# Kernel tuning notes

Measured on AMD Instinct MI355X. Metric: run time of the kernel, lower is better.

Reference implementation:

```python
import jax, jax.numpy as jnp
import numpy as np
from jax import lax

N, D, K = 8192, 512, 16
EPS = 1e-8


def _safe_sqrt(x):
    # sqrt with a guard so vjp is finite at exact zeros (diagonal of dist matrix)
    return jnp.where(x > 0, jnp.sqrt(jnp.maximum(x, 1e-12)), 0.0)


def _pairwise_dist(a):
    # [n, d] -> [n, n] euclidean distances via Gram trick
    sq = jnp.sum(a * a, axis=-1)
    d2 = sq[:, None] + sq[None, :] - 2.0 * (a @ a.T)
    return _safe_sqrt(d2)


def _curvature_proxy(emb, k):
    n = emb.shape[0]
    dists = _pairwise_dist(emb)  # [n, n]
    neg_d, knn_idx = lax.top_k(-dists, k + 1)  # k+1 smallest
    knn_dists = -neg_d[:, 1:]   # drop self [n, k]
    knn_idx = knn_idx[:, 1:]    # [n, k]
    avg_dist_to_neighbors = knn_dists.mean(axis=1)  # [n]

    nb = emb[knn_idx]  # [n, k, d] gathered neighbor embeddings
    nsq = jnp.sum(nb * nb, axis=-1)  # [n, k]
    gram = jnp.einsum('nkd,nld->nkl', nb, nb)  # [n, k, k]
    inter = _safe_sqrt(nsq[:, :, None] + nsq[:, None, :] - 2.0 * gram)

    mask = jnp.triu(jnp.ones((k, k), dtype=bool), 1)
    n_pairs = k * (k - 1) // 2
    inter_mean = jnp.sum(jnp.where(mask, inter, 0.0), axis=(1, 2)) / n_pairs  # [n]

    curvature = inter_mean / (avg_dist_to_neighbors + EPS)
    return curvature, knn_dists


def setup_inputs() -> dict:
    key = jax.random.key(0)
    k1, k2, k3 = jax.random.split(key, 3)
    embeddings = jax.random.normal(k1, (N, D), dtype=jnp.float32)
    ref_curvature = jax.random.uniform(k2, (N,), dtype=jnp.float32)
    ref_distances = jax.random.uniform(k3, (N, K), dtype=jnp.float32)
    return {"embeddings": embeddings, "ref_curvature": ref_curvature,
            "ref_distances": ref_distances}


def reference(embeddings, ref_curvature, ref_distances):
    curr_curv, curr_dists = _curvature_proxy(embeddings, K)
    curvature_loss = jnp.mean((curr_curv - ref_curvature) ** 2)
    scale_loss = (curr_dists.mean() - ref_distances.mean()) ** 2
    return curvature_loss + 0.1 * scale_loss
```

## Files before the change

### kernel.cpp

```cpp
#include <hip/hip_runtime.h>
#include <cfloat>
#include <cmath>
#include <stdint.h>

#define N 8192
#define D 512
#define K 16
#define RB 64
#define JS 2048
#define NSL (N / JS)
#define JT 128
#define KC 64
#define NCH (D / KC)
#define CAP 32
#define PB 64

typedef __bf16 bf16x8 __attribute__((ext_vector_type(8)));
typedef __bf16 bf16x4 __attribute__((ext_vector_type(4)));
typedef float  f32x16 __attribute__((ext_vector_type(16)));
typedef float  f32x4  __attribute__((ext_vector_type(4)));

__global__ __launch_bounds__(256)
void k_cast_sqnorm(const float* __restrict__ emb, float* __restrict__ sq,
                   __bf16* __restrict__ embh) {
    int row = blockIdx.x * 4 + (threadIdx.x >> 6);
    int lane = threadIdx.x & 63;
    const float4* e = (const float4*)(emb + (size_t)row * D);
    float s = 0.f;
    #pragma unroll
    for (int c = 0; c < 2; c++) {
        float4 v = e[lane + 64 * c];
        s += v.x * v.x + v.y * v.y + v.z * v.z + v.w * v.w;
        bf16x4 h = { (__bf16)v.x, (__bf16)v.y, (__bf16)v.z, (__bf16)v.w };
        *(bf16x4*)&embh[(size_t)row * D + (size_t)(lane + 64 * c) * 4] = h;
    }
    for (int off = 32; off; off >>= 1) s += __shfl_down(s, off, 64);
    if (lane == 0) sq[row] = s;
}

__global__ __launch_bounds__(512)
void k_knn(const __bf16* __restrict__ embh, const float* __restrict__ sq,
           float* __restrict__ pd2, int* __restrict__ pidx) {
    __shared__ __align__(16) __bf16 As[2][RB][KC + 8];
    __shared__ __align__(16) __bf16 Bs[2][JT][KC + 8];
    __shared__ float svD[RB][CAP + 1];
    __shared__ int   svI[RB][CAP + 1];
    __shared__ float sqr[RB];
    __shared__ float kadj[RB];
    __shared__ int   scount[RB];
    __shared__ int   again;

    const int t   = threadIdx.x;
    const int rg  = blockIdx.x >> 2;
    const int sl  = blockIdx.x & 3;
    const int ib  = rg * RB;
    const int jsb = sl * JS;
    const int lane = t & 63, quad = lane >> 5, l31 = lane & 31;
    const int w  = t >> 6;
    const int wr = (w & 1) * 32;
    const int wc = (w >> 1) * 32;

    const int mrow = t >> 3, tid8 = t & 7;
    float l0 = FLT_MAX, l1 = FLT_MAX;
    int   i0 = 0, i1 = 0;
    float kmx = FLT_MAX;

    if (t < RB) {
        sqr[t] = sq[ib + t];
        kadj[t] = FLT_MAX; scount[t] = 0;
    }
    __syncthreads();

    for (int jt = 0; jt < JS / JT; jt++) {
        const int jb = jsb + jt * JT;
        f32x16 acc = {};

        {
            int row = t >> 3, g = t & 7;
            *(uint4*)&As[0][row][g * 8] = *(const uint4*)&embh[(size_t)(ib + row) * D + g * 8];
            #pragma unroll
            for (int q = 0; q < 2; q++) {
                int s = t + 512 * q;
                int brow = s >> 3, bg = s & 7;
                *(uint4*)&Bs[0][brow][bg * 8] = *(const uint4*)&embh[(size_t)(jb + brow) * D + bg * 8];
            }
        }
        __syncthreads();

        uint4 pfA, pfB[2];
        for (int kc = 0; kc < NCH; kc++) {
            const int cur = kc & 1;
            if (kc + 1 < NCH) {
                int k0 = (kc + 1) * KC;
                {
                    int row = t >> 3, g = t & 7;
                    pfA = *(const uint4*)&embh[(size_t)(ib + row) * D + k0 + g * 8];
                }
                #pragma unroll
                for (int q = 0; q < 2; q++) {
                    int s = t + 512 * q; int brow = s >> 3, bg = s & 7;
                    pfB[q] = *(const uint4*)&embh[(size_t)(jb + brow) * D + k0 + bg * 8];
                }
            }
            #pragma unroll
            for (int kk = 0; kk < KC / 16; kk++) {
                int ko = kk * 16 + quad * 8;
                bf16x8 a0 = *(const bf16x8*)&As[cur][wr + l31][ko];
                bf16x8 b0 = *(const bf16x8*)&Bs[cur][wc + l31][ko];
                acc = __builtin_amdgcn_mfma_f32_32x32x16_bf16(a0, b0, acc, 0, 0, 0);
            }
            if (kc + 1 < NCH) {
                {
                    int row = t >> 3, g = t & 7;
                    *(uint4*)&As[cur ^ 1][row][g * 8] = pfA;
                }
                #pragma unroll
                for (int q = 0; q < 2; q++) {
                    int s = t + 512 * q; int brow = s >> 3, bg = s & 7;
                    *(uint4*)&Bs[cur ^ 1][brow][bg * 8] = pfB[q];
                }
            }
            __syncthreads();
        }

        float sqc0 = sq[jb + wc + l31];
        uint32_t mask = 0;
        while (true) {
            if (t == 0) again = 0;
            #pragma unroll
            for (int reg = 0; reg < 16; reg++) {
                if ((mask >> reg) & 1) continue;
                int row_l = wr + ((reg & 3) + ((reg >> 2) << 3) + (quad << 2));
                float t2 = sqc0 - 2.f * acc[reg];
                if (t2 < kadj[row_l]) {
                    int j = jb + wc + l31;
                    if (j != ib + row_l) {
                        int p = atomicAdd(&scount[row_l], 1);
                        if (p < CAP) {
                            svD[row_l][p] = t2 + sqr[row_l];
                            svI[row_l][p] = j;
                            mask |= (1u << reg);
                        }
                    }
                }
            }
            __syncthreads();
            {
                int cnt = scount[mrow];
                if (cnt) {
                    int m = cnt < CAP ? cnt : CAP;
                    for (int p = 0; p < m; p++) {
                        float d2 = svD[mrow][p];
                        if (d2 < kmx) {
                            float mx = l0; int am = 0;
                            if (l1 > mx) { mx = l1; am = 1; }
                            int gam = (tid8 << 1) | am;
                            #pragma unroll
                            for (int off = 1; off < 8; off <<= 1) {
                                float omx = __shfl_xor(mx, off, 64);
                                int   oga = __shfl_xor(gam, off, 64);
                                if (omx > mx || (omx == mx && oga < gam)) { mx = omx; gam = oga; }
                            }
                            if ((gam >> 1) == tid8) {
                                int jv = svI[mrow][p];
                                if ((gam & 1) == 0) { l0 = d2; i0 = jv; }
                                else                { l1 = d2; i1 = jv; }
                            }
                            float lm = fmaxf(l0, l1);
                            #pragma unroll
                            for (int off = 1; off < 8; off <<= 1)
                                lm = fmaxf(lm, __shfl_xor(lm, off, 64));
                            kmx = lm;
                        }
                    }
                    if (tid8 == 0) {
                        kadj[mrow] = kmx - sqr[mrow];
                        scount[mrow] = 0;
                        if (cnt > CAP) again = 1;
                    }
                }
            }
            __syncthreads();
            int more = again;
            __syncthreads();
            if (!more) break;
        }
    }

    {
        size_t base = (size_t)(ib + mrow) * (NSL * K) + sl * K + tid8 * 2;
        pd2[base + 0] = l0; pd2[base + 1] = l1;
        pidx[base + 0] = i0; pidx[base + 1] = i1;
    }
}

__global__ __launch_bounds__(256)
void k_merge(const float* __restrict__ pd2, const int* __restrict__ pidx,
             int* __restrict__ knn, float* __restrict__ row_sum) {
    int row = blockIdx.x * 256 + threadIdx.x;
    float bd[K]; int bi[K];
    #pragma unroll
    for (int q = 0; q < K; q++) { bd[q] = FLT_MAX; bi[q] = 0; }
    float kmx = FLT_MAX;
    const float* pr = pd2 + (size_t)row * (NSL * K);
    const int*   pi = pidx + (size_t)row * (NSL * K);
    for (int s = 0; s < NSL * K; s++) {
        float d2 = pr[s];
        if (d2 < kmx) {
            int am = 0; float mx = bd[0];
            #pragma unroll
            for (int q = 1; q < K; q++) if (bd[q] > mx) { mx = bd[q]; am = q; }
            bd[am] = d2; bi[am] = pi[s];
            mx = bd[0];
            #pragma unroll
            for (int q = 1; q < K; q++) mx = fmaxf(mx, bd[q]);
            kmx = mx;
        }
    }
    float s = 0.f;
    #pragma unroll
    for (int q = 0; q < K; q++) {
        float d2 = bd[q];
        s += (d2 > 0.f) ? sqrtf(fmaxf(d2, 1e-12f)) : 0.f;
        knn[(size_t)row * K + q] = bi[q];
    }
    row_sum[row] = s;
}

__global__ __launch_bounds__(256)
void k_curv(const __bf16* __restrict__ embh, const int* __restrict__ knn_idx,
            const float* __restrict__ row_sum, const float* __restrict__ ref_curv,
            float* __restrict__ curv_err) {
    __shared__ float diagS[4][16];
    const int t = threadIdx.x;
    const int w = t >> 6, lane = t & 63;
    const int i = blockIdx.x * 4 + w;

    const int nidx = knn_idx[(size_t)i * K + (lane & 15)];
    const __bf16* src = embh + (size_t)nidx * D + (lane >> 4) * 8;

    f32x4 acc = {};
    #pragma unroll
    for (int kc = 0; kc < D / 32; kc++) {
        bf16x8 a = *(const bf16x8*)(src + kc * 32);
        acc = __builtin_amdgcn_mfma_f32_16x16x32_bf16(a, a, acc, 0, 0, 0);
    }

    #pragma unroll
    for (int q = 0; q < 4; q++) {
        int r = (lane >> 4) * 4 + q;
        if (r == (lane & 15)) diagS[w][r] = acc[q];
    }
    __syncthreads();

    float s = 0.f;
    #pragma unroll
    for (int q = 0; q < 4; q++) {
        int r = (lane >> 4) * 4 + q, c = lane & 15;
        if (r != c) {
            float d2 = diagS[w][r] + diagS[w][c] - 2.f * acc[q];
            s += (d2 > 0.f) ? sqrtf(fmaxf(d2, 1e-12f)) : 0.f;
        }
    }
    #pragma unroll
    for (int off = 32; off; off >>= 1) s += __shfl_down(s, off, 64);

    if (lane == 0) {
        float inter_mean = (0.5f * s) / 120.f;
        float avg = row_sum[i] / 16.f;
        float curv = inter_mean / (avg + 1e-8f);
        float diff = curv - ref_curv[i];
        curv_err[i] = diff * diff;
    }
}

__global__ __launch_bounds__(256)
void k_part(const float* __restrict__ curv_err, const float* __restrict__ row_sum,
            const float* __restrict__ ref_dist, float* __restrict__ part) {
    const int b = blockIdx.x, t = threadIdx.x;
    const int gid = b * 256 + t;
    const int stride = PB * 256;
    float s1 = 0.f, s2 = 0.f, s3 = 0.f;
    for (int i = gid; i < N; i += stride) { s1 += curv_err[i]; s2 += row_sum[i]; }
    for (int i = gid; i < N * K; i += stride) s3 += ref_dist[i];
    for (int off = 32; off; off >>= 1) {
        s1 += __shfl_down(s1, off, 64);
        s2 += __shfl_down(s2, off, 64);
        s3 += __shfl_down(s3, off, 64);
    }
    __shared__ float a1[4], a2[4], a3[4];
    int w = t >> 6, lane = t & 63;
    if (lane == 0) { a1[w] = s1; a2[w] = s2; a3[w] = s3; }
    __syncthreads();
    if (t == 0) {
        float t1 = 0.f, t2 = 0.f, t3 = 0.f;
        #pragma unroll
        for (int q = 0; q < 4; q++) { t1 += a1[q]; t2 += a2[q]; t3 += a3[q]; }
        part[b] = t1; part[PB + b] = t2; part[2 * PB + b] = t3;
    }
}

__global__ __launch_bounds__(64)
void k_final2(const float* __restrict__ part, float* __restrict__ out) {
    const int t = threadIdx.x;
    float s1 = part[t], s2 = part[PB + t], s3 = part[2 * PB + t];
    for (int off = 32; off; off >>= 1) {
        s1 += __shfl_down(s1, off, 64);
        s2 += __shfl_down(s2, off, 64);
        s3 += __shfl_down(s3, off, 64);
    }
    if (t == 0) {
        float curv_loss = s1 / (float)N;
        float dm = s2 / (float)(N * K);
        float rm = s3 / (float)(N * K);
        float d = dm - rm;
        out[0] = curv_loss + 0.1f * d * d;
    }
}

extern "C" void kernel_launch(void* const* d_in, const int* in_sizes, int n_in,
                              void* d_out, int out_size, void* d_ws, size_t ws_size,
                              hipStream_t stream) {
    const float* emb      = (const float*)d_in[0];
    const float* ref_curv = (const float*)d_in[1];
    const float* ref_dist = (const float*)d_in[2];
    float* out = (float*)d_out;

    float*  sq       = (float*)d_ws;
    float*  row_sum  = sq + N;
    float*  curv_err = row_sum + N;
    float*  pd2      = curv_err + N;
    int*    pidx     = (int*)(pd2 + (size_t)N * NSL * K);
    int*    knn      = pidx + (size_t)N * NSL * K;
    __bf16* embh     = (__bf16*)(knn + (size_t)N * K);
    float*  part     = (float*)(embh + (size_t)N * D);

    k_cast_sqnorm<<<N / 4, 256, 0, stream>>>(emb, sq, embh);
    k_knn<<<(N / RB) * NSL, 512, 0, stream>>>(embh, sq, pd2, pidx);
    k_merge<<<N / 256, 256, 0, stream>>>(pd2, pidx, knn, row_sum);
    k_curv<<<N / 4, 256, 0, stream>>>(embh, knn, row_sum, ref_curv, curv_err);
    k_part<<<PB, 256, 0, stream>>>(curv_err, row_sum, ref_dist, part);
    k_final2<<<1, 64, 0, stream>>>(part, out);
}
```

Baseline: 386.0 us.

## Use direct global-to-LDS loads with XOR-swizzled tiles and cross-tile prefetch

Replaces the register-staged global loads and LDS stores in the kNN GEMM with global_load_lds direct transfers into shared memory. The padded LDS layout becomes an XOR-swizzled layout to avoid bank conflicts, and the double buffer now prefetches the first chunk of the next column tile during the last chunk of the current one, which removes the per-tile prologue barrier. This cuts register pressure and VALU/LDS store instructions. It relies on the wave-uniform LDS base plus lane offset semantics of global_load_lds being matched exactly by the swizzle, and on the single barrier per chunk being enough to order the async LDS writes.

```diff
diff --git a/kernel.cpp b/kernel.cpp
--- a/kernel.cpp
+++ b/kernel.cpp
@@ -10,6 +10,7 @@
 #define JS 2048
 #define NSL (N / JS)
 #define JT 128
+#define NT (JS / JT)
 #define KC 64
 #define NCH (D / KC)
 #define CAP 32
@@ -19,6 +20,12 @@
 typedef __bf16 bf16x4 __attribute__((ext_vector_type(4)));
 typedef float  f32x16 __attribute__((ext_vector_type(16)));
 typedef float  f32x4  __attribute__((ext_vector_type(4)));
+
+__device__ __forceinline__ void gl2lds(const __bf16* g, void* l) {
+    __builtin_amdgcn_global_load_lds(
+        (const __attribute__((address_space(1))) void*)g,
+        (__attribute__((address_space(3))) void*)l, 16, 0, 0);
+}
 
 __global__ __launch_bounds__(256)
 void k_cast_sqnorm(const float* __restrict__ emb, float* __restrict__ sq,
@@ -41,8 +48,8 @@
 __global__ __launch_bounds__(512)
 void k_knn(const __bf16* __restrict__ embh, const float* __restrict__ sq,
            float* __restrict__ pd2, int* __restrict__ pidx) {
-    __shared__ __align__(16) __bf16 As[2][RB][KC + 8];
-    __shared__ __align__(16) __bf16 Bs[2][JT][KC + 8];
+    __shared__ __align__(16) __bf16 As[2][RB][KC];
+    __shared__ __align__(16) __bf16 Bs[2][JT][KC];
     __shared__ float svD[RB][CAP + 1];
     __shared__ int   svI[RB][CAP + 1];
     __shared__ float sqr[RB];
@@ -59,6 +66,9 @@
     const int w  = t >> 6;
     const int wr = (w & 1) * 32;
     const int wc = (w >> 1) * 32;
+    const int xr = l31 & 7;
+
+    const int st_arow = t >> 3, st_ag = (t & 7) ^ (st_arow & 7);
 
     const int mrow = t >> 3, tid8 = t & 7;
     float l0 = FLT_MAX, l1 = FLT_MAX;
@@ -69,58 +79,46 @@
         sqr[t] = sq[ib + t];
         kadj[t] = FLT_MAX; scount[t] = 0;
     }
+
+    gl2lds(&embh[(size_t)(ib + st_arow) * D + (st_ag << 3)],
+           (char*)&As[0][0][0] + w * 1024);
+    #pragma unroll
+    for (int q = 0; q < 2; q++) {
+        int s2 = t + 512 * q; int brow = s2 >> 3, bg = (s2 & 7) ^ (brow & 7);
+        gl2lds(&embh[(size_t)(jsb + brow) * D + (bg << 3)],
+               (char*)&Bs[0][0][0] + q * 8192 + w * 1024);
+    }
     __syncthreads();
 
-    for (int jt = 0; jt < JS / JT; jt++) {
+    int cb = 0;
+    for (int jt = 0; jt < NT; jt++) {
         const int jb = jsb + jt * JT;
         f32x16 acc = {};
 
-        {
-            int row = t >> 3, g = t & 7;
-            *(uint4*)&As[0][row][g * 8] = *(const uint4*)&embh[(size_t)(ib + row) * D + g * 8];
-            #pragma unroll
-            for (int q = 0; q < 2; q++) {
-                int s = t + 512 * q;
-                int brow = s >> 3, bg = s & 7;
-                *(uint4*)&Bs[0][brow][bg * 8] = *(const uint4*)&embh[(size_t)(jb + brow) * D + bg * 8];
-            }
-        }
-        __syncthreads();
-
-        uint4 pfA, pfB[2];
         for (int kc = 0; kc < NCH; kc++) {
-            const int cur = kc & 1;
-            if (kc + 1 < NCH) {
-                int k0 = (kc + 1) * KC;
-                {
-                    int row = t >> 3, g = t & 7;
-                    pfA = *(const uint4*)&embh[(size_t)(ib + row) * D + k0 + g * 8];
-                }
+            if (kc + 1 < NCH || jt + 1 < NT) {
+                const int nk0 = (kc + 1 < NCH) ? (kc + 1) * KC : 0;
+                const int njb = (kc + 1 < NCH) ? jb : jb + JT;
+                gl2lds(&embh[(size_t)(ib + st_arow) * D + nk0 + (st_ag << 3)],
+                       (char*)&As[cb ^ 1][0][0] + w * 1024);
                 #pragma unroll
                 for (int q = 0; q < 2; q++) {
-                    int s = t + 512 * q; int brow = s >> 3, bg = s & 7;
-                    pfB[q] = *(const uint4*)&embh[(size_t)(jb + brow) * D + k0 + bg * 8];
+                    int s2 = t + 512 * q; int brow = s2 >> 3, bg = (s2 & 7) ^ (brow & 7);
+                    gl2lds(&embh[(size_t)(njb + brow) * D + nk0 + (bg << 3)],
+                           (char*)&Bs[cb ^ 1][0][0] + q * 8192 + w * 1024);
                 }
             }
+            const char* abase = (const char*)&As[cb][0][0];
+            const char* bbase = (const char*)&Bs[cb][0][0];
             #pragma unroll
             for (int kk = 0; kk < KC / 16; kk++) {
-                int ko = kk * 16 + quad * 8;
-                bf16x8 a0 = *(const bf16x8*)&As[cur][wr + l31][ko];
-                bf16x8 b0 = *(const bf16x8*)&Bs[cur][wc + l31][ko];
+                int gi = (kk << 1) | quad;
+                bf16x8 a0 = *(const bf16x8*)(abase + (wr + l31) * 128 + ((gi ^ xr) << 4));
+                bf16x8 b0 = *(const bf16x8*)(bbase + (wc + l31) * 128 + ((gi ^ xr) << 4));
                 acc = __builtin_amdgcn_mfma_f32_32x32x16_bf16(a0, b0, acc, 0, 0, 0);
             }
-            if (kc + 1 < NCH) {
-                {
-                    int row = t >> 3, g = t & 7;
-                    *(uint4*)&As[cur ^ 1][row][g * 8] = pfA;
-                }
-                #pragma unroll
-                for (int q = 0; q < 2; q++) {
-                    int s = t + 512 * q; int brow = s >> 3, bg = s & 7;
-                    *(uint4*)&Bs[cur ^ 1][brow][bg * 8] = pfB[q];
-                }
-            }
             __syncthreads();
+            cb ^= 1;
         }
 
         float sqc0 = sq[jb + wc + l31];
```

Measured after the change: 408.2 us. +5.8%, slower.

## Share kNN pruning threshold across column-slice blocks via global atomicMin

Applied to the files above, without the earlier changes.

Adds a global per-row k-th distance bound that each column-slice block updates with atomicMin and reads before candidate filtering, so blocks working on other slices of the same row can prune candidates earlier. It also fills the first K candidates directly without the shuffle-based max search, and double-buffers the retry flag to drop one barrier per pass. The cost is extra global atomics and reads per tile, and a dependence on cross-block timing. Correctness relies on the shared bound being a valid upper bound, which holds because each slice's top-K max bounds the global k-th distance.

```diff
diff --git a/kernel.cpp b/kernel.cpp
--- a/kernel.cpp
+++ b/kernel.cpp
@@ -10,6 +10,7 @@
 #define JS 2048
 #define NSL (N / JS)
 #define JT 128
+#define NT (JS / JT)
 #define KC 64
 #define NCH (D / KC)
 #define CAP 32
@@ -22,7 +23,7 @@
 
 __global__ __launch_bounds__(256)
 void k_cast_sqnorm(const float* __restrict__ emb, float* __restrict__ sq,
-                   __bf16* __restrict__ embh) {
+                   __bf16* __restrict__ embh, int* __restrict__ kadjG) {
     int row = blockIdx.x * 4 + (threadIdx.x >> 6);
     int lane = threadIdx.x & 63;
     const float4* e = (const float4*)(emb + (size_t)row * D);
@@ -36,11 +37,13 @@
     }
     for (int off = 32; off; off >>= 1) s += __shfl_down(s, off, 64);
     if (lane == 0) sq[row] = s;
+    if (lane == 1) kadjG[row] = 0x7f7fffff;
 }
 
 __global__ __launch_bounds__(512)
 void k_knn(const __bf16* __restrict__ embh, const float* __restrict__ sq,
-           float* __restrict__ pd2, int* __restrict__ pidx) {
+           float* __restrict__ pd2, int* __restrict__ pidx,
+           int* __restrict__ kadjG) {
     __shared__ __align__(16) __bf16 As[2][RB][KC + 8];
     __shared__ __align__(16) __bf16 Bs[2][JT][KC + 8];
     __shared__ float svD[RB][CAP + 1];
@@ -48,7 +51,7 @@
     __shared__ float sqr[RB];
     __shared__ float kadj[RB];
     __shared__ int   scount[RB];
-    __shared__ int   again;
+    __shared__ int   again2[2];
 
     const int t   = threadIdx.x;
     const int rg  = blockIdx.x >> 2;
@@ -64,6 +67,7 @@
     float l0 = FLT_MAX, l1 = FLT_MAX;
     int   i0 = 0, i1 = 0;
     float kmx = FLT_MAX;
+    int   nfill = 0;
 
     if (t < RB) {
         sqr[t] = sq[ib + t];
@@ -71,7 +75,7 @@
     }
     __syncthreads();
 
-    for (int jt = 0; jt < JS / JT; jt++) {
+    for (int jt = 0; jt < NT; jt++) {
         const int jb = jsb + jt * JT;
         f32x16 acc = {};
 
@@ -123,10 +127,17 @@
             __syncthreads();
         }
 
+        if (t < RB) {
+            float g = __int_as_float(kadjG[ib + t]);
+            kadj[t] = fminf(kadj[t], g - sqr[t]);
+        }
+        if (t == 0) again2[0] = 0;
+        __syncthreads();
+
         float sqc0 = sq[jb + wc + l31];
         uint32_t mask = 0;
+        int pass = 0;
         while (true) {
-            if (t == 0) again = 0;
             #pragma unroll
             for (int reg = 0; reg < 16; reg++) {
                 if ((mask >> reg) & 1) continue;
@@ -152,39 +163,58 @@
                     for (int p = 0; p < m; p++) {
                         float d2 = svD[mrow][p];
                         if (d2 < kmx) {
-                            float mx = l0; int am = 0;
-                            if (l1 > mx) { mx = l1; am = 1; }
-                            int gam = (tid8 << 1) | am;
-                            #pragma unroll
-                            for (int off = 1; off < 8; off <<= 1) {
-                                float omx = __shfl_xor(mx, off, 64);
-                                int   oga = __shfl_xor(gam, off, 64);
-                                if (omx > mx || (omx == mx && oga < gam)) { mx = omx; gam = oga; }
+                            if (nfill < K) {
+                                if ((nfill >> 1) == tid8) {
+                                    int jv = svI[mrow][p];
+                                    if ((nfill & 1) == 0) { l0 = d2; i0 = jv; }
+                                    else                  { l1 = d2; i1 = jv; }
+                                }
+                                nfill++;
+                                if (nfill == K) {
+                                    float lm = fmaxf(l0, l1);
+                                    #pragma unroll
+                                    for (int off = 1; off < 8; off <<= 1)
+                                        lm = fmaxf(lm, __shfl_xor(lm, off, 64));
+                                    kmx = lm;
+                                }
+                            } else {
+                                float mx = l0; int am = 0;
+                                if (l1 > mx) { mx = l1; am = 1; }
+                                int gam = (tid8 << 1) | am;
+                                #pragma unroll
+                                for (int off = 1; off < 8; off <<= 1) {
+                                    float omx = __shfl_xor(mx, off, 64);
+                                    int   oga = __shfl_xor(gam, off, 64);
+                                    if (omx > mx || (omx == mx && oga < gam)) { mx = omx; gam = oga; }
+                                }
+                                if ((gam >> 1) == tid8) {
+                                    int jv = svI[mrow][p];
+                                    if ((gam & 1) == 0) { l0 = d2; i0 = jv; }
+                                    else                { l1 = d2; i1 = jv; }
+                                }
+                                float lm = fmaxf(l0, l1);
+                                #pragma unroll
+                                for (int off = 1; off < 8; off <<= 1)
+                                    lm = fmaxf(lm, __shfl_xor(lm, off, 64));
+                                kmx = lm;
                             }
-                            if ((gam >> 1) == tid8) {
-                                int jv = svI[mrow][p];
-                                if ((gam & 1) == 0) { l0 = d2; i0 = jv; }
-                                else                { l1 = d2; i1 = jv; }
-                            }
-                            float lm = fmaxf(l0, l1);
-                            #pragma unroll
-                            for (int off = 1; off < 8; off <<= 1)
-                                lm = fmaxf(lm, __shfl_xor(lm, off, 64));
-                            kmx = lm;
                         }
                     }
                     if (tid8 == 0) {
-                        kadj[mrow] = kmx - sqr[mrow];
+                        kadj[mrow] = fminf(kadj[mrow], kmx - sqr[mrow]);
                         scount[mrow] = 0;
-                        if (cnt > CAP) again = 1;
+                        if (cnt > CAP) again2[pass & 1] = 1;
                     }
                 }
             }
+            if (t == 0) again2[(pass + 1) & 1] = 0;
             __syncthreads();
-            int more = again;
-            __syncthreads();
-            if (!more) break;
-        }
+            if (!again2[pass & 1]) break;
+            pass++;
+        }
+
+        if (tid8 == 0 && kmx < FLT_MAX)
+            atomicMin(&kadjG[ib + mrow], __float_as_int(kmx));
     }
 
     {
@@ -334,9 +364,10 @@
     int*    knn      = pidx + (size_t)N * NSL * K;
     __bf16* embh     = (__bf16*)(knn + (size_t)N * K);
     float*  part     = (float*)(embh + (size_t)N * D);
-
-    k_cast_sqnorm<<<N / 4, 256, 0, stream>>>(emb, sq, embh);
-    k_knn<<<(N / RB) * NSL, 512, 0, stream>>>(embh, sq, pd2, pidx);
+    int*    kadjG    = (int*)(part + 3 * PB);
+
+    k_cast_sqnorm<<<N / 4, 256, 0, stream>>>(emb, sq, embh, kadjG);
+    k_knn<<<(N / RB) * NSL, 512, 0, stream>>>(embh, sq, pd2, pidx, kadjG);
     k_merge<<<N / 256, 256, 0, stream>>>(pd2, pidx, knn, row_sum);
     k_curv<<<N / 4, 256, 0, stream>>>(embh, knn, row_sum, ref_curv, curv_err);
     k_part<<<PB, 256, 0, stream>>>(curv_err, row_sum, ref_dist, part);
```

New measurement: 369.3 us. 4.3% less time.
